# Performance work log

Measured on AMD Instinct MI355X. Metric: run time of the kernel, lower is better.

The kernel has to match this reference:

```python
import jax, jax.numpy as jnp
import numpy as np

N_NODES = 20000
N_EDGES = 100000
WIDTH = 64
KER_IN = 6
KER_HID = WIDTH // 4  # 16
DEPTH = 6


def setup_inputs() -> dict:
    key = jax.random.key(0)
    ks = jax.random.split(key, 12)
    s = lambda fan_in: 1.0 / np.sqrt(fan_in)
    return {
        "x": jax.random.normal(ks[0], (N_NODES, 1), dtype=jnp.float32),
        "edge_index": jax.random.randint(ks[1], (2, N_EDGES), 0, N_NODES, dtype=jnp.int32),
        "edge_attr": jax.random.uniform(ks[2], (N_EDGES, KER_IN), dtype=jnp.float32),
        "fc1_w": jax.random.normal(ks[3], (1, WIDTH), dtype=jnp.float32) * s(1),
        "fc1_b": jnp.zeros((WIDTH,), dtype=jnp.float32),
        "k1_w": jax.random.normal(ks[4], (KER_IN, KER_HID), dtype=jnp.float32) * s(KER_IN),
        "k1_b": jnp.zeros((KER_HID,), dtype=jnp.float32),
        "k2_w": jax.random.normal(ks[5], (KER_HID, WIDTH * WIDTH), dtype=jnp.float32) * s(KER_HID),
        "k2_b": jnp.zeros((WIDTH * WIDTH,), dtype=jnp.float32),
        "root_w": jax.random.normal(ks[6], (WIDTH, WIDTH), dtype=jnp.float32) * s(WIDTH),
        "conv_b": jnp.zeros((WIDTH,), dtype=jnp.float32),
        "fc2_w": jax.random.normal(ks[7], (WIDTH, 1), dtype=jnp.float32) * s(WIDTH),
        "fc2_b": jnp.zeros((1,), dtype=jnp.float32),
    }


def reference(x, edge_index, edge_attr, fc1_w, fc1_b, k1_w, k1_b, k2_w, k2_b,
              root_w, conv_b, fc2_w, fc2_b):
    src = edge_index[0]  # source nodes j
    dst = edge_index[1]  # target nodes i

    # fc1: lift node features [N,1] -> [N,W]
    h = x @ fc1_w + fc1_b

    # Edge-conditioned weight matrices via kernel MLP (edge_attr is layer-invariant,
    # so compute once and reuse for all DEPTH layers — identical math).
    ek = jax.nn.relu(edge_attr @ k1_w + k1_b)           # [E, W/4]
    W = (ek @ k2_w + k2_b).reshape(N_EDGES, WIDTH, WIDTH)  # [E, W, W]

    # mean aggregation denominator (in-degree, clamped to avoid div-by-zero)
    deg = jax.ops.segment_sum(jnp.ones((N_EDGES,), dtype=h.dtype), dst,
                              num_segments=N_NODES)
    denom = jnp.maximum(deg, 1.0)[:, None]               # [N,1]

    for _ in range(DEPTH):
        # per-edge matmul: msg_e = x_src[e] @ W_e
        msg = jnp.einsum('ei,eio->eo', h[src], W)        # [E, W]
        agg = jax.ops.segment_sum(msg, dst, num_segments=N_NODES) / denom
        h = jax.nn.relu(agg + h @ root_w + conv_b)       # NNConv root weight + bias, then outer ReLU

    return h @ fc2_w + fc2_b                              # [N, 1]
```

## Files before the change

kernel.cpp:

```cpp
#include <hip/hip_runtime.h>
#include <hip/hip_bf16.h>


#define NN 20000
#define NE 100000
#define WD 64
#define DEPTH 6
#define TM 12
#define LSTR 1092

typedef __attribute__((ext_vector_type(8))) short bf16x8;
typedef __attribute__((ext_vector_type(4))) float f32x4;

__device__ __forceinline__ unsigned short f2bf(float v) {
    union { float f; unsigned u; } x; x.f = v;
    unsigned r = x.u + 0x7fffu + ((x.u >> 16) & 1u);
    return (unsigned short)(r >> 16);
}
__device__ __forceinline__ float bf2f(unsigned short b) {
    union { unsigned u; float f; } x; x.u = ((unsigned)b) << 16;
    return x.f;
}

__global__ __launch_bounds__(256) void count_kernel(const int* __restrict__ ei,
                                                    int* __restrict__ outc,
                                                    int* __restrict__ inc)
{
    int e = blockIdx.x * 256 + threadIdx.x;
    if (e >= NE) return;
    atomicAdd(&outc[ei[e]], 1);
    atomicAdd(&inc[ei[NE + e]], 1);
}

__global__ __launch_bounds__(256) void scanA_kernel(const int* __restrict__ cnt,
                                                    int* __restrict__ partials)
{
    int b = blockIdx.x, t = threadIdx.x, lane = t & 63, w = t >> 6;
    int base = b * 1024 + t * 4;
    int s = 0;
#pragma unroll
    for (int i = 0; i < 4; ++i) {
        int idx = base + i;
        if (idx < 2 * NN) s += cnt[idx];
    }
#pragma unroll
    for (int off = 32; off > 0; off >>= 1) s += __shfl_down(s, off, 64);
    __shared__ int wsum[4];
    if (lane == 0) wsum[w] = s;
    __syncthreads();
    if (t == 0) partials[b] = wsum[0] + wsum[1] + wsum[2] + wsum[3];
}

__global__ __launch_bounds__(64) void scanB_kernel(const int* __restrict__ partials,
                                                   int* __restrict__ bases)
{
    int l = threadIdx.x;
    int p = (l < 40) ? partials[l] : 0;
    int v = p;
#pragma unroll
    for (int off = 1; off < 64; off <<= 1) {
        int u = __shfl_up(v, off, 64);
        if (l >= off) v += u;
    }
    if (l < 40) bases[l] = v - p;
}

__global__ __launch_bounds__(256) void scanC_kernel(const int* __restrict__ cnt,
                                                    const int* __restrict__ bases,
                                                    int* __restrict__ rps,
                                                    int* __restrict__ rpd,
                                                    float* __restrict__ invd)
{
    int b = blockIdx.x, t = threadIdx.x, lane = t & 63, w = t >> 6;
    int base = b * 1024 + t * 4;
    int v[4], s = 0;
#pragma unroll
    for (int i = 0; i < 4; ++i) {
        int idx = base + i;
        v[i] = (idx < 2 * NN) ? cnt[idx] : 0;
        s += v[i];
    }
    int tsum = s, sc = s;
#pragma unroll
    for (int off = 1; off < 64; off <<= 1) {
        int u = __shfl_up(sc, off, 64);
        if (lane >= off) sc += u;
    }
    __shared__ int wtot[4];
    if (lane == 63) wtot[w] = sc;
    __syncthreads();
    int wbase = 0;
    for (int j = 0; j < w; ++j) wbase += wtot[j];
    int run = bases[b] + wbase + sc - tsum;
#pragma unroll
    for (int i = 0; i < 4; ++i) {
        int idx = base + i;
        int e = run; run += v[i];
        if (idx < NN) {
            rps[idx] = e;
        } else if (idx < 2 * NN) {
            rpd[idx - NN] = e - NE;
            invd[idx - NN] = 1.0f / fmaxf((float)v[i], 1.0f);
        }
    }
    if (b == 0 && t == 0) { rps[NN] = NE; rpd[NN] = NE; }
}

__global__ __launch_bounds__(256) void ekfill_kernel(
    const int* __restrict__ ei, const float* __restrict__ ea,
    const float* __restrict__ k1w, const float* __restrict__ k1b,
    const int* __restrict__ rps, const int* __restrict__ rpd,
    int* __restrict__ fs, int* __restrict__ fd,
    float* __restrict__ eks, int* __restrict__ sdmeta)
{
    int e = blockIdx.x * 256 + threadIdx.x;
    if (e >= NE) return;
    int s = ei[e], d = ei[NE + e];
    float a[6];
#pragma unroll
    for (int i = 0; i < 6; ++i) a[i] = ea[e * 6 + i];
    int slot_s = rps[s] + atomicAdd(&fs[s], 1);
    int slot_d = rpd[d] + atomicAdd(&fd[d], 1);
    sdmeta[2 * slot_s]     = slot_d;
    sdmeta[2 * slot_s + 1] = s;
#pragma unroll
    for (int j = 0; j < 16; ++j) {
        float v = k1b[j];
#pragma unroll
        for (int i = 0; i < 6; ++i) v = fmaf(a[i], k1w[i * 16 + j], v);
        eks[(size_t)slot_s * 16 + j] = fmaxf(v, 0.f);
    }
}

__global__ __launch_bounds__(256) void gwt_kernel(
    const float* __restrict__ k2w, const float* __restrict__ k2b,
    const float* __restrict__ rootw,
    unsigned short* __restrict__ Gh, unsigned short* __restrict__ Gl)
{
    int idx = blockIdx.x * 256 + threadIdx.x;
    if (idx >= 1152 * 64) return;
    int n = idx >> 6, k = idx & 63;
    int b = n >> 6, o = n & 63;
    float g;
    if (b < 16)       g = k2w[b * 4096 + k * 64 + o];
    else if (b == 16) g = k2b[k * 64 + o];
    else              g = rootw[k * 64 + o];
    unsigned short hi = f2bf(g);
    Gh[idx] = hi;
    Gl[idx] = f2bf(g - bf2f(hi));
}

__global__ __launch_bounds__(256) void h0_kernel(
    const float* __restrict__ x, const float* __restrict__ w,
    const float* __restrict__ b,
    unsigned short* __restrict__ hhi, unsigned short* __restrict__ hlo)
{
    int idx = blockIdx.x * 256 + threadIdx.x;
    if (idx >= NN * WD) return;
    int n = idx >> 6, o = idx & 63;
    float v = fmaf(x[n], w[o], b[o]);
    unsigned short hi = f2bf(v);
    hhi[idx] = hi;
    hlo[idx] = f2bf(v - bf2f(hi));
}

__global__ __launch_bounds__(512, 6) void fused_kernel(
    const unsigned short* __restrict__ hhi, const unsigned short* __restrict__ hlo,
    const unsigned short* __restrict__ Gh, const unsigned short* __restrict__ Gl,
    const float* __restrict__ eks, const int* __restrict__ sdmeta,
    const int* __restrict__ rps, float* __restrict__ Proot,
    float* __restrict__ msg)
{
    __shared__ __align__(16) float Pt[TM * LSTR];
    __shared__ int rb[TM + 1];
    int n0 = blockIdx.x * TM;
    int w = threadIdx.x >> 6, l = threadIdx.x & 63;
    int quad = l >> 4, lr = l & 15;
    if (threadIdx.x < TM + 1) {
        int gi = n0 + threadIdx.x;
        rb[threadIdx.x] = rps[gi > NN ? NN : gi];
    }
    int arow = n0 + lr;
    if (arow > NN - 1) arow = NN - 1;
    const bf16x8* pah = (const bf16x8*)(hhi + (size_t)arow * 64 + quad * 8);
    const bf16x8* pal = (const bf16x8*)(hlo + (size_t)arow * 64 + quad * 8);
    bf16x8 ah0 = pah[0], ah1 = pah[4];
    bf16x8 al0 = pal[0], al1 = pal[4];

    for (int st = w; st < 18; st += 8) {
        f32x4 acc[4];
#pragma unroll
        for (int t = 0; t < 4; ++t) acc[t] = (f32x4){0.f, 0.f, 0.f, 0.f};
#pragma unroll
        for (int t = 0; t < 4; ++t) {
            int brow = st * 64 + t * 16 + lr;
            const bf16x8* pbh = (const bf16x8*)(Gh + (size_t)brow * 64 + quad * 8);
            const bf16x8* pbl = (const bf16x8*)(Gl + (size_t)brow * 64 + quad * 8);
            bf16x8 bh0 = pbh[0], bh1 = pbh[4];
            bf16x8 bl0 = pbl[0], bl1 = pbl[4];
            f32x4 a = acc[t];
            a = __builtin_amdgcn_mfma_f32_16x16x32_bf16(ah0, bh0, a, 0, 0, 0);
            a = __builtin_amdgcn_mfma_f32_16x16x32_bf16(ah0, bl0, a, 0, 0, 0);
            a = __builtin_amdgcn_mfma_f32_16x16x32_bf16(al0, bh0, a, 0, 0, 0);
            a = __builtin_amdgcn_mfma_f32_16x16x32_bf16(ah1, bh1, a, 0, 0, 0);
            a = __builtin_amdgcn_mfma_f32_16x16x32_bf16(ah1, bl1, a, 0, 0, 0);
            a = __builtin_amdgcn_mfma_f32_16x16x32_bf16(al1, bh1, a, 0, 0, 0);
            acc[t] = a;
        }
        if (st < 17) {
#pragma unroll
            for (int t = 0; t < 4; ++t)
#pragma unroll
                for (int r = 0; r < 4; ++r) {
                    int row = quad * 4 + r;
                    if (row < TM)
                        Pt[row * LSTR + st * 64 + t * 16 + lr] = acc[t][r];
                }
        } else {
#pragma unroll
            for (int t = 0; t < 4; ++t)
#pragma unroll
                for (int r = 0; r < 4; ++r) {
                    int row = quad * 4 + r;
                    int gn = n0 + row;
                    if (row < TM && gn < NN)
                        Proot[(size_t)gn * 64 + t * 16 + lr] = acc[t][r];
                }
        }
    }
    __syncthreads();

    int nend = n0 + TM; if (nend > NN) nend = NN;
    int r0 = rb[0], r1 = rb[nend - n0];
    int total = r1 - r0;
    if (total <= 0) return;
    int per = (total + 7) >> 3;
    int s0 = r0 + w * per;
    int s1 = s0 + per; if (s1 > r1) s1 = r1;
    if (s0 >= s1) return;

    float p[17];
    int lnp = -1;
    int su = __builtin_amdgcn_readfirstlane(s0);
    const float* er = eks + (size_t)su * 16;
    f32x4 e0 = *(const f32x4*)(er);
    f32x4 e1 = *(const f32x4*)(er + 4);
    f32x4 e2 = *(const f32x4*)(er + 8);
    f32x4 e3 = *(const f32x4*)(er + 12);
    int ds  = sdmeta[2 * su];
    int src = sdmeta[2 * su + 1];

    for (int s = s0; s < s1; ++s) {
        f32x4 c0 = e0, c1 = e1, c2 = e2, c3 = e3;
        int cds = ds, cln = src - n0;
        if (s + 1 < s1) {
            int su2 = __builtin_amdgcn_readfirstlane(s + 1);
            const float* er2 = eks + (size_t)su2 * 16;
            e0 = *(const f32x4*)(er2);
            e1 = *(const f32x4*)(er2 + 4);
            e2 = *(const f32x4*)(er2 + 8);
            e3 = *(const f32x4*)(er2 + 12);
            ds  = sdmeta[2 * su2];
            src = sdmeta[2 * su2 + 1];
        }
        if (cln != lnp) {
            const float* Pr = &Pt[cln * LSTR];
#pragma unroll
            for (int k = 0; k < 17; ++k) p[k] = Pr[k * 64 + l];
            lnp = cln;
        }
        float ma = p[16], mb = 0.f;
        ma = fmaf(c0[0], p[0], ma);  mb = fmaf(c0[1], p[1], mb);
        ma = fmaf(c0[2], p[2], ma);  mb = fmaf(c0[3], p[3], mb);
        ma = fmaf(c1[0], p[4], ma);  mb = fmaf(c1[1], p[5], mb);
        ma = fmaf(c1[2], p[6], ma);  mb = fmaf(c1[3], p[7], mb);
        ma = fmaf(c2[0], p[8], ma);  mb = fmaf(c2[1], p[9], mb);
        ma = fmaf(c2[2], p[10], ma); mb = fmaf(c2[3], p[11], mb);
        ma = fmaf(c3[0], p[12], ma); mb = fmaf(c3[1], p[13], mb);
        ma = fmaf(c3[2], p[14], ma); mb = fmaf(c3[3], p[15], mb);
        msg[(size_t)cds * 64 + l] = ma + mb;
    }
}

__global__ __launch_bounds__(256) void agg_kernel(
    const float* __restrict__ msg, const int* __restrict__ rpd,
    const float* __restrict__ invd, const float* __restrict__ Proot,
    const float* __restrict__ convb, float* __restrict__ h,
    unsigned short* __restrict__ hhi, unsigned short* __restrict__ hlo)
{
    int i = blockIdx.x * 4 + (threadIdx.x >> 6);
    if (i >= NN) return;
    int l = threadIdx.x & 63;
    int r0 = rpd[i], r1 = rpd[i + 1];
    float a0 = 0.f, a1 = 0.f, a2 = 0.f, a3 = 0.f;
    int s = r0;
    for (; s + 3 < r1; s += 4) {
        a0 += msg[(size_t)s * 64 + l];
        a1 += msg[(size_t)(s + 1) * 64 + l];
        a2 += msg[(size_t)(s + 2) * 64 + l];
        a3 += msg[(size_t)(s + 3) * 64 + l];
    }
    for (; s < r1; ++s) a0 += msg[(size_t)s * 64 + l];
    float acc = (a0 + a1) + (a2 + a3);
    float v = fmaf(acc, invd[i], Proot[(size_t)i * 64 + l] + convb[l]);
    v = fmaxf(v, 0.f);
    int idx = i * 64 + l;
    h[idx] = v;
    unsigned short hi = f2bf(v);
    hhi[idx] = hi;
    hlo[idx] = f2bf(v - bf2f(hi));
}

__global__ __launch_bounds__(256) void out_kernel(
    const float* __restrict__ h, const float* __restrict__ fc2_w,
    const float* __restrict__ fc2_b, float* __restrict__ out)
{
    int wave = blockIdx.x * 4 + (threadIdx.x >> 6);
    int lane = threadIdx.x & 63;
    float v = h[(size_t)wave * 64 + lane] * fc2_w[lane];
#pragma unroll
    for (int off = 32; off > 0; off >>= 1) v += __shfl_down(v, off);
    if (lane == 0) out[wave] = v + fc2_b[0];
}

extern "C" void kernel_launch(void* const* d_in, const int* in_sizes, int n_in,
                              void* d_out, int out_size, void* d_ws, size_t ws_size,
                              hipStream_t stream)
{
    const float* x         = (const float*)d_in[0];
    const int*   ei        = (const int*)  d_in[1];
    const float* edge_attr = (const float*)d_in[2];
    const float* fc1_w     = (const float*)d_in[3];
    const float* fc1_b     = (const float*)d_in[4];
    const float* k1_w      = (const float*)d_in[5];
    const float* k1_b      = (const float*)d_in[6];
    const float* k2_w      = (const float*)d_in[7];
    const float* k2_b      = (const float*)d_in[8];
    const float* root_w    = (const float*)d_in[9];
    const float* conv_b    = (const float*)d_in[10];
    const float* fc2_w     = (const float*)d_in[11];
    const float* fc2_b     = (const float*)d_in[12];
    float* out = (float*)d_out;

    float* ws = (float*)d_ws;
    size_t off = 0;
    int* cnt   = (int*)(ws + off); off += 4 * NN;
    int* outc  = cnt;
    int* inc   = cnt + NN;
    int* fs    = cnt + 2 * NN;
    int* fd    = cnt + 3 * NN;
    int* rps   = (int*)(ws + off); off += 20004;
    int* rpd   = (int*)(ws + off); off += 20004;
    int* partials = (int*)(ws + off); off += 64;
    int* bases    = (int*)(ws + off); off += 64;
    int* sdmeta   = (int*)(ws + off); off += 2 * NE + 16;
    float* invd  = ws + off; off += NN;
    float* eks   = ws + off; off += (size_t)NE * 16;
    unsigned short* Gh  = (unsigned short*)(ws + off); off += 36864;
    unsigned short* Gl  = (unsigned short*)(ws + off); off += 36864;
    unsigned short* hhi = (unsigned short*)(ws + off); off += (size_t)NN * 32;
    unsigned short* hlo = (unsigned short*)(ws + off); off += (size_t)NN * 32;
    float* h     = ws + off; off += (size_t)NN * WD;
    float* msg   = ws + off; off += (size_t)NE * WD;
    float* Proot = ws + off; off += (size_t)NN * WD;

    hipMemsetAsync(cnt, 0, 4 * NN * sizeof(int), stream);
    count_kernel<<<(NE + 255) / 256, 256, 0, stream>>>(ei, outc, inc);
    scanA_kernel<<<40, 256, 0, stream>>>(cnt, partials);
    scanB_kernel<<<1, 64, 0, stream>>>(partials, bases);
    scanC_kernel<<<40, 256, 0, stream>>>(cnt, bases, rps, rpd, invd);
    ekfill_kernel<<<(NE + 255) / 256, 256, 0, stream>>>(ei, edge_attr, k1_w, k1_b,
                                                        rps, rpd, fs, fd, eks, sdmeta);
    gwt_kernel<<<(1152 * 64 + 255) / 256, 256, 0, stream>>>(k2_w, k2_b, root_w, Gh, Gl);
    h0_kernel<<<(NN * WD + 255) / 256, 256, 0, stream>>>(x, fc1_w, fc1_b, hhi, hlo);

    int ntiles = (NN + TM - 1) / TM;
    for (int layer = 0; layer < DEPTH; ++layer) {
        fused_kernel<<<ntiles, 512, 0, stream>>>(hhi, hlo, Gh, Gl, eks, sdmeta,
                                                 rps, Proot, msg);
        agg_kernel<<<(NN + 3) / 4, 256, 0, stream>>>(msg, rpd, invd, Proot,
                                                     conv_b, h, hhi, hlo);
    }

    out_kernel<<<NN / 4, 256, 0, stream>>>(h, fc2_w, fc2_b, out);
}
```

Measured before the change: 597.4 us.

## Split fused node GEMM and edge contraction into separate kernels via global P buffer

Replaces the fused kernel, which kept a 12-node slice of the per-node projection in LDS, with two kernels. A 64-row-tile MFMA GEMM writes the full projection P to global memory, possibly in chunks sized to the workspace, and an edge kernel assigns one wave per source node to read its P row once and loop over its edges. This is meant to improve MFMA tile utilization and lift the LDS occupancy limit. In exchange each layer writes and reads roughly 87 MB of P through global memory or L2, and launches more kernels. The source-node metadata per edge is also dropped.

```diff
diff --git a/kernel.cpp b/kernel.cpp
--- a/kernel.cpp
+++ b/kernel.cpp
@@ -6,8 +6,7 @@
 #define NE 100000
 #define WD 64
 #define DEPTH 6
-#define TM 12
-#define LSTR 1092
+#define BM 64
 
 typedef __attribute__((ext_vector_type(8))) short bf16x8;
 typedef __attribute__((ext_vector_type(4))) float f32x4;
@@ -121,8 +120,7 @@
     for (int i = 0; i < 6; ++i) a[i] = ea[e * 6 + i];
     int slot_s = rps[s] + atomicAdd(&fs[s], 1);
     int slot_d = rpd[d] + atomicAdd(&fd[d], 1);
-    sdmeta[2 * slot_s]     = slot_d;
-    sdmeta[2 * slot_s + 1] = s;
+    sdmeta[slot_s] = slot_d;
 #pragma unroll
     for (int j = 0; j < 16; ++j) {
         float v = k1b[j];
@@ -164,30 +162,25 @@
     hlo[idx] = f2bf(v - bf2f(hi));
 }
 
-__global__ __launch_bounds__(512, 6) void fused_kernel(
+__global__ __launch_bounds__(512) void pgemm_kernel(
     const unsigned short* __restrict__ hhi, const unsigned short* __restrict__ hlo,
     const unsigned short* __restrict__ Gh, const unsigned short* __restrict__ Gl,
-    const float* __restrict__ eks, const int* __restrict__ sdmeta,
-    const int* __restrict__ rps, float* __restrict__ Proot,
-    float* __restrict__ msg)
-{
-    __shared__ __align__(16) float Pt[TM * LSTR];
-    __shared__ int rb[TM + 1];
-    int n0 = blockIdx.x * TM;
+    float* __restrict__ P, float* __restrict__ Proot,
+    int nbase, int nend)
+{
+    int n0 = nbase + blockIdx.x * BM;
     int w = threadIdx.x >> 6, l = threadIdx.x & 63;
     int quad = l >> 4, lr = l & 15;
-    if (threadIdx.x < TM + 1) {
-        int gi = n0 + threadIdx.x;
-        rb[threadIdx.x] = rps[gi > NN ? NN : gi];
-    }
-    int arow = n0 + lr;
-    if (arow > NN - 1) arow = NN - 1;
-    const bf16x8* pah = (const bf16x8*)(hhi + (size_t)arow * 64 + quad * 8);
-    const bf16x8* pal = (const bf16x8*)(hlo + (size_t)arow * 64 + quad * 8);
-    bf16x8 ah0 = pah[0], ah1 = pah[4];
-    bf16x8 al0 = pal[0], al1 = pal[4];
-
-    for (int st = w; st < 18; st += 8) {
+
+    for (int T = w; T < 72; T += 8) {
+        int rg = T / 18, st = T % 18;
+        int arow = n0 + rg * 16 + lr;
+        if (arow > NN - 1) arow = NN - 1;
+        const bf16x8* pah = (const bf16x8*)(hhi + (size_t)arow * 64 + quad * 8);
+        const bf16x8* pal = (const bf16x8*)(hlo + (size_t)arow * 64 + quad * 8);
+        bf16x8 ah0 = pah[0], ah1 = pah[4];
+        bf16x8 al0 = pal[0], al1 = pal[4];
+
         f32x4 acc[4];
 #pragma unroll
         for (int t = 0; t < 4; ++t) acc[t] = (f32x4){0.f, 0.f, 0.f, 0.f};
@@ -212,62 +205,60 @@
             for (int t = 0; t < 4; ++t)
 #pragma unroll
                 for (int r = 0; r < 4; ++r) {
-                    int row = quad * 4 + r;
-                    if (row < TM)
-                        Pt[row * LSTR + st * 64 + t * 16 + lr] = acc[t][r];
+                    int gn = n0 + rg * 16 + quad * 4 + r;
+                    if (gn < nend)
+                        P[(size_t)(gn - nbase) * 1088 + st * 64 + t * 16 + lr]
+                            = acc[t][r];
                 }
         } else {
 #pragma unroll
             for (int t = 0; t < 4; ++t)
 #pragma unroll
                 for (int r = 0; r < 4; ++r) {
-                    int row = quad * 4 + r;
-                    int gn = n0 + row;
-                    if (row < TM && gn < NN)
+                    int gn = n0 + rg * 16 + quad * 4 + r;
+                    if (gn < nend)
                         Proot[(size_t)gn * 64 + t * 16 + lr] = acc[t][r];
                 }
         }
     }
-    __syncthreads();
-
-    int nend = n0 + TM; if (nend > NN) nend = NN;
-    int r0 = rb[0], r1 = rb[nend - n0];
-    int total = r1 - r0;
-    if (total <= 0) return;
-    int per = (total + 7) >> 3;
-    int s0 = r0 + w * per;
-    int s1 = s0 + per; if (s1 > r1) s1 = r1;
-    if (s0 >= s1) return;
-
+}
+
+__global__ __launch_bounds__(256, 6) void edgec_kernel(
+    const float* __restrict__ P, const float* __restrict__ eks,
+    const int* __restrict__ sdmeta, const int* __restrict__ rps,
+    float* __restrict__ msg, int nbase, int nend)
+{
+    int wv = __builtin_amdgcn_readfirstlane(threadIdx.x >> 6);
+    int n = nbase + blockIdx.x * 4 + wv;
+    if (n >= nend) return;
+    int l = threadIdx.x & 63;
+    int r0 = rps[n], r1 = rps[n + 1];
+    if (r0 >= r1) return;
+
+    const float* Pr = P + (size_t)(n - nbase) * 1088;
     float p[17];
-    int lnp = -1;
-    int su = __builtin_amdgcn_readfirstlane(s0);
+#pragma unroll
+    for (int k = 0; k < 17; ++k) p[k] = Pr[k * 64 + l];
+
+    int su = __builtin_amdgcn_readfirstlane(r0);
     const float* er = eks + (size_t)su * 16;
     f32x4 e0 = *(const f32x4*)(er);
     f32x4 e1 = *(const f32x4*)(er + 4);
     f32x4 e2 = *(const f32x4*)(er + 8);
     f32x4 e3 = *(const f32x4*)(er + 12);
-    int ds  = sdmeta[2 * su];
-    int src = sdmeta[2 * su + 1];
-
-    for (int s = s0; s < s1; ++s) {
+    int ds = sdmeta[su];
+
+    for (int s = r0; s < r1; ++s) {
         f32x4 c0 = e0, c1 = e1, c2 = e2, c3 = e3;
-        int cds = ds, cln = src - n0;
-        if (s + 1 < s1) {
-            int su2 = __builtin_amdgcn_readfirstlane(s + 1);
-            const float* er2 = eks + (size_t)su2 * 16;
+        int cds = ds;
+        if (s + 1 < r1) {
+            int s2 = __builtin_amdgcn_readfirstlane(s + 1);
+            const float* er2 = eks + (size_t)s2 * 16;
             e0 = *(const f32x4*)(er2);
             e1 = *(const f32x4*)(er2 + 4);
             e2 = *(const f32x4*)(er2 + 8);
             e3 = *(const f32x4*)(er2 + 12);
-            ds  = sdmeta[2 * su2];
-            src = sdmeta[2 * su2 + 1];
-        }
-        if (cln != lnp) {
-            const float* Pr = &Pt[cln * LSTR];
-#pragma unroll
-            for (int k = 0; k < 17; ++k) p[k] = Pr[k * 64 + l];
-            lnp = cln;
+            ds = sdmeta[s2];
         }
         float ma = p[16], mb = 0.f;
         ma = fmaf(c0[0], p[0], ma);  mb = fmaf(c0[1], p[1], mb);
@@ -353,7 +344,7 @@
     int* rpd   = (int*)(ws + off); off += 20004;
     int* partials = (int*)(ws + off); off += 64;
     int* bases    = (int*)(ws + off); off += 64;
-    int* sdmeta   = (int*)(ws + off); off += 2 * NE + 16;
+    int* sdmeta   = (int*)(ws + off); off += NE + 16;
     float* invd  = ws + off; off += NN;
     float* eks   = ws + off; off += (size_t)NE * 16;
     unsigned short* Gh  = (unsigned short*)(ws + off); off += 36864;
@@ -363,6 +354,14 @@
     float* h     = ws + off; off += (size_t)NN * WD;
     float* msg   = ws + off; off += (size_t)NE * WD;
     float* Proot = ws + off; off += (size_t)NN * WD;
+    float* P     = ws + off;
+
+    size_t totalf = ws_size / sizeof(float);
+    size_t availf = totalf > off ? totalf - off : 0;
+    int nch = 1;
+    if (availf < (size_t)NN * 1088)            nch = 2;
+    if (nch == 2 && availf < (size_t)(NN / 2) * 1088) nch = 4;
+    int csz = NN / nch;
 
     hipMemsetAsync(cnt, 0, 4 * NN * sizeof(int), stream);
     count_kernel<<<(NE + 255) / 256, 256, 0, stream>>>(ei, outc, inc);
@@ -374,10 +373,14 @@
     gwt_kernel<<<(1152 * 64 + 255) / 256, 256, 0, stream>>>(k2_w, k2_b, root_w, Gh, Gl);
     h0_kernel<<<(NN * WD + 255) / 256, 256, 0, stream>>>(x, fc1_w, fc1_b, hhi, hlo);
 
-    int ntiles = (NN + TM - 1) / TM;
     for (int layer = 0; layer < DEPTH; ++layer) {
-        fused_kernel<<<ntiles, 512, 0, stream>>>(hhi, hlo, Gh, Gl, eks, sdmeta,
-                                                 rps, Proot, msg);
+        for (int c = 0; c < nch; ++c) {
+            int nb = c * csz, ne = nb + csz;
+            pgemm_kernel<<<(csz + BM - 1) / BM, 512, 0, stream>>>(
+                hhi, hlo, Gh, Gl, P, Proot, nb, ne);
+            edgec_kernel<<<(csz + 3) / 4, 256, 0, stream>>>(
+                P, eks, sdmeta, rps, msg, nb, ne);
+        }
         agg_kernel<<<(NN + 3) / 4, 256, 0, stream>>>(msg, rpd, invd, Proot,
                                                      conv_b, h, hhi, hlo);
     }
```

Result: slower. 858.6 us (+43.7%).
